# Kernel tuning notes

Measured on AMD Instinct MI355X. Metric: run time of the kernel, lower is better.

The kernel has to match this reference:

```python
import jax, jax.numpy as jnp
import numpy as np

B, P, D, H, U, C = 32, 196, 512, 8, 4, 500

def setup_inputs() -> dict:
    key = jax.random.key(0)
    ks = jax.random.split(key, 12)
    s = 0.02
    return {
        "patch_embeddings": jax.random.normal(ks[0], (B, P, D), jnp.float32),
        "global_features": jax.random.normal(ks[1], (B, D), jnp.float32),
        "query_vectors": jax.random.normal(ks[2], (H, D), jnp.float32) * s,
        "dom_W": jax.random.normal(ks[3], (D, D), jnp.float32) / np.sqrt(D),
        "dom_b": jnp.zeros((D,), jnp.float32),
        "sem_W": jax.random.normal(ks[4], (H, D, D), jnp.float32) / np.sqrt(D),
        "sem_b": jnp.zeros((H, D), jnp.float32),
        "unknown_semantic_tokens": jax.random.normal(ks[5], (U, D), jnp.float32) * s,
        "known_prefix": jax.random.normal(ks[6], (C, 1, D), jnp.float32) * s,   # SOS embedding per class
        "known_suffix": jax.random.normal(ks[7], (C, 1, D), jnp.float32) * s,   # last-token embedding per class
        "unk_prefix": jax.random.normal(ks[8], (1, D), jnp.float32) * s,
        "unk_suffix": jax.random.normal(ks[9], (1, D), jnp.float32) * s,
    }


def reference(patch_embeddings, global_features, query_vectors, dom_W, dom_b,
              sem_W, sem_b, unknown_semantic_tokens, known_prefix, known_suffix,
              unk_prefix, unk_suffix):
    b, p, d = patch_embeddings.shape
    h = query_vectors.shape[0]
    c = known_prefix.shape[0]
    u = unknown_semantic_tokens.shape[0]

    # SemanticTokenExtractor: per-head attention over patches (vectorized over heads)
    scores = jnp.einsum('bpd,hd->bph', patch_embeddings, query_vectors)      # [B,P,H]
    weights = jax.nn.softmax(scores, axis=1)                                  # softmax over patches
    semantic_tokens = jnp.einsum('bph,bpd->bhd', weights, patch_embeddings)   # [B,H,D]

    # DomainTokenGenerator (2D input -> identity) + domain projection (torch Linear: x @ W.T + b)
    projected_domain = global_features @ dom_W.T + dom_b                      # [B,D]

    # Per-head semantic projections: head k uses its own Linear
    projected_sem = jnp.einsum('bhd,hed->bhe', semantic_tokens, sem_W) + sem_b  # [B,H,D]

    # Known prompts: for each (b, c): [prefix_c(1), domain_b(1), semantics_b(H), suffix_c(1)]
    pre = jnp.broadcast_to(known_prefix[None], (b, c, 1, d))
    dom = jnp.broadcast_to(projected_domain[:, None, None, :], (b, c, 1, d))
    sem = jnp.broadcast_to(projected_sem[:, None], (b, c, h, d))
    suf = jnp.broadcast_to(known_suffix[None], (b, c, 1, d))
    known_prompts = jnp.concatenate([pre, dom, sem, suf], axis=2).reshape(b * c, h + 3, d)

    # Unknown prompts: [unk_prefix(1), domain_b(1), unknown_semantic_tokens(U), unk_suffix(1)]
    upre = jnp.broadcast_to(unk_prefix[None], (b, 1, d))
    udom = projected_domain[:, None, :]
    usem = jnp.broadcast_to(unknown_semantic_tokens[None], (b, u, d))
    usuf = jnp.broadcast_to(unk_suffix[None], (b, 1, d))
    unknown_prompts = jnp.concatenate([upre, udom, usem, usuf], axis=1)       # [B, U+3, D]

    return known_prompts, unknown_prompts, semantic_tokens
```

## Files before the change

kernel.cpp:

```cpp
#include <hip/hip_runtime.h>

typedef unsigned int uint32;
typedef uint32 v4u __attribute__((ext_vector_type(4)));

#define Bb 32
#define Pp 196
#define Dd 512
#define Hh 8
#define Uu 4
#define Cc 500

#define OUT1_ELEM_OFF 90112000
#define OUT2_ELEM_OFF 90226688

#define NPC 16

#define WS_SC   0
#define WS_PART 51200
#define WS_DOM  2148352
#define WS_SEM  2164736

__device__ __forceinline__ float dot4(float4 a, float4 b, float acc) {
    acc = fmaf(a.x, b.x, acc);
    acc = fmaf(a.y, b.y, acc);
    acc = fmaf(a.z, b.z, acc);
    acc = fmaf(a.w, b.w, acc);
    return acc;
}

__global__ __launch_bounds__(256)
void k_scores(const float* __restrict__ patch, const float* __restrict__ query,
              float* __restrict__ sc) {
    __shared__ float s_q[Hh * Dd];
    const int b = blockIdx.x / 49;
    const int p0 = (blockIdx.x % 49) * 4;
    const int tid = threadIdx.x;
    for (int j = tid; j < Hh * Dd / 4; j += 256)
        ((float4*)s_q)[j] = ((const float4*)query)[j];
    __syncthreads();

    const int wave = tid >> 6, lane = tid & 63;
    const int p = p0 + wave;
    const float* pr = patch + ((size_t)b * Pp + p) * Dd + lane * 8;
    const float4 v0 = *(const float4*)pr;
    const float4 v1 = *(const float4*)(pr + 4);

    float out = 0.f;
#pragma unroll
    for (int h = 0; h < 8; ++h) {
        const float4 q0 = *(const float4*)&s_q[h * Dd + lane * 8];
        const float4 q1 = *(const float4*)&s_q[h * Dd + lane * 8 + 4];
        float a = dot4(v0, q0, 0.f);
        a = dot4(v1, q1, a);
#pragma unroll
        for (int m = 32; m >= 1; m >>= 1) a += __shfl_xor(a, m, 64);
        if (lane == h) out = a;
    }
    if (lane < 8) sc[((size_t)b * Hh + lane) * Pp + p] = out;
}

__global__ __launch_bounds__(256)
void k_pool_part(const float* __restrict__ patch, const float* __restrict__ sc,
                 float* __restrict__ part) {
    __shared__ float s_w[Hh * Pp];
    const int b = blockIdx.x >> 4;
    const int pc = blockIdx.x & 15;
    const int tid = threadIdx.x;

    for (int j = tid; j < Hh * Pp; j += 256) s_w[j] = sc[(size_t)b * Hh * Pp + j];
    __syncthreads();

    {
        const int h = tid >> 5, gl = tid & 31;
        float m = -1e30f;
        for (int p = gl; p < Pp; p += 32) m = fmaxf(m, s_w[h * Pp + p]);
#pragma unroll
        for (int mm = 16; mm >= 1; mm >>= 1) m = fmaxf(m, __shfl_xor(m, mm, 64));
        float s = 0.f;
        for (int p = gl; p < Pp; p += 32) s += __expf(s_w[h * Pp + p] - m);
#pragma unroll
        for (int mm = 16; mm >= 1; mm >>= 1) s += __shfl_xor(s, mm, 64);
        const float inv = 1.f / s;
        for (int p = gl; p < Pp; p += 32)
            s_w[h * Pp + p] = __expf(s_w[h * Pp + p] - m) * inv;
    }
    __syncthreads();

    const int f = tid & 127;
    const int hq = tid >> 7;
    const int pstart = pc * 13;
    const int pend = (pstart + 13 < Pp) ? pstart + 13 : Pp;
    float4 a0 = {0, 0, 0, 0}, a1 = a0, a2 = a0, a3 = a0;
    const float4* pb4 = (const float4*)(patch + (size_t)b * Pp * Dd);
    for (int p = pstart; p < pend; ++p) {
        const float4 pv = pb4[p * 128 + f];
        const float w0 = s_w[(hq * 4 + 0) * Pp + p];
        const float w1 = s_w[(hq * 4 + 1) * Pp + p];
        const float w2 = s_w[(hq * 4 + 2) * Pp + p];
        const float w3 = s_w[(hq * 4 + 3) * Pp + p];
        a0.x = fmaf(w0, pv.x, a0.x); a0.y = fmaf(w0, pv.y, a0.y);
        a0.z = fmaf(w0, pv.z, a0.z); a0.w = fmaf(w0, pv.w, a0.w);
        a1.x = fmaf(w1, pv.x, a1.x); a1.y = fmaf(w1, pv.y, a1.y);
        a1.z = fmaf(w1, pv.z, a1.z); a1.w = fmaf(w1, pv.w, a1.w);
        a2.x = fmaf(w2, pv.x, a2.x); a2.y = fmaf(w2, pv.y, a2.y);
        a2.z = fmaf(w2, pv.z, a2.z); a2.w = fmaf(w2, pv.w, a2.w);
        a3.x = fmaf(w3, pv.x, a3.x); a3.y = fmaf(w3, pv.y, a3.y);
        a3.z = fmaf(w3, pv.z, a3.z); a3.w = fmaf(w3, pv.w, a3.w);
    }
    float4* po = (float4*)part + ((size_t)b * NPC + pc) * 1024;
    po[(hq * 4 + 0) * 128 + f] = a0;
    po[(hq * 4 + 1) * 128 + f] = a1;
    po[(hq * 4 + 2) * 128 + f] = a2;
    po[(hq * 4 + 3) * 128 + f] = a3;
}

__global__ __launch_bounds__(256)
void k_combine(const float* __restrict__ part, float* __restrict__ st) {
    const int idx = blockIdx.x * 256 + threadIdx.x;
    const int b = idx >> 10;
    const int r = idx & 1023;
    const float4* p4 = (const float4*)part;
    float4 a = {0, 0, 0, 0};
#pragma unroll
    for (int pc = 0; pc < NPC; ++pc) {
        const float4 v = p4[((size_t)b * NPC + pc) * 1024 + r];
        a.x += v.x; a.y += v.y; a.z += v.z; a.w += v.w;
    }
    ((float4*)st)[idx] = a;
}

#define PJS 513
__global__ __launch_bounds__(256)
void k_proj(const float* __restrict__ gf, const float* __restrict__ domW,
            const float* __restrict__ domb, const float* __restrict__ semW,
            const float* __restrict__ semb, const float* __restrict__ st,
            float* __restrict__ dom_ws, float* __restrict__ sem_ws) {
    __shared__ float s_w[32 * PJS];
    __shared__ float s_st[32 * PJS];
    const int blk = blockIdx.x;
    const int tid = threadIdx.x;
    if (blk < 128) {
        const int h = blk >> 4;
        const int e0 = (blk & 15) * 32;
        for (int g = tid; g < 32 * 128; g += 256) {
            const int r = g >> 7, c4 = g & 127;
            const float4 w = ((const float4*)semW)[((size_t)(h * Dd + e0 + r)) * 128 + c4];
            float* dw = &s_w[r * PJS + c4 * 4];
            dw[0] = w.x; dw[1] = w.y; dw[2] = w.z; dw[3] = w.w;
            const float4 s = ((const float4*)st)[((size_t)(r * Hh + h)) * 128 + c4];
            float* ds = &s_st[r * PJS + c4 * 4];
            ds[0] = s.x; ds[1] = s.y; ds[2] = s.z; ds[3] = s.w;
        }
        __syncthreads();
        const int pe = tid & 15;
        const int pb = tid >> 4;
        const float* w0r = &s_w[(2 * pe) * PJS];
        const float* w1r = &s_w[(2 * pe + 1) * PJS];
        const float* s0r = &s_st[(2 * pb) * PJS];
        const float* s1r = &s_st[(2 * pb + 1) * PJS];
        float a00 = 0.f, a01 = 0.f, a10 = 0.f, a11 = 0.f;
#pragma unroll 8
        for (int d = 0; d < Dd; ++d) {
            const float w0 = w0r[d], w1 = w1r[d];
            const float s0 = s0r[d], s1 = s1r[d];
            a00 = fmaf(s0, w0, a00);
            a01 = fmaf(s0, w1, a01);
            a10 = fmaf(s1, w0, a10);
            a11 = fmaf(s1, w1, a11);
        }
        const int e_ = e0 + 2 * pe;
        const float b0 = semb[h * Dd + e_], b1 = semb[h * Dd + e_ + 1];
        float* o0 = &sem_ws[((2 * pb) * Hh + h) * Dd + e_];
        float* o1 = &sem_ws[((2 * pb + 1) * Hh + h) * Dd + e_];
        o0[0] = a00 + b0; o0[1] = a01 + b1;
        o1[0] = a10 + b0; o1[1] = a11 + b1;
    } else {
        const int tg = (blk - 128) * 256 + tid;
        const int b = tg >> 9;
        const int e = tg & 511;
        const float4* wr = (const float4*)(domW + (size_t)e * Dd);
        const float4* gr = (const float4*)(gf + (size_t)b * Dd);
        float acc = domb[e];
#pragma unroll 8
        for (int j = 0; j < Dd / 4; ++j) acc = dot4(gr[j], wr[j], acc);
        dom_ws[b * Dd + e] = acc;
    }
}

__global__ __launch_bounds__(256)
void k_assemble(const v4u* __restrict__ pre, const v4u* __restrict__ suf,
                const v4u* __restrict__ dom, const v4u* __restrict__ sem,
                const v4u* __restrict__ upre, const v4u* __restrict__ usuf,
                const v4u* __restrict__ ust,
                v4u* __restrict__ out0, v4u* __restrict__ out1) {
    const int blk = blockIdx.x;
    const int tid = threadIdx.x;
    if (blk < 16000) {
        const int b = blk / 500;
        const int c = blk % 500;
        v4u* row = out0 + (size_t)blk * 1408;
#pragma unroll
        for (int k = 0; k < 6; ++k) {
            const int i = tid + k * 256;
            if (k < 5 || i < 1408) {
                const int t = i >> 7;
                const int off = i & 127;
                v4u v;
                if (t == 0) v = pre[c * 128 + off];
                else if (t == 10) v = suf[c * 128 + off];
                else if (t == 1) v = dom[b * 128 + off];
                else v = sem[b * 1024 + (t - 2) * 128 + off];
                row[i] = v;
            }
        }
    } else {
        const int b = blk - 16000;
#pragma unroll
        for (int k = 0; k < 4; ++k) {
            const int i = tid + k * 256;
            if (k < 3 || i < 896) {
                const int t = i >> 7;
                const int off = i & 127;
                v4u v;
                if (t == 0) v = upre[off];
                else if (t == 6) v = usuf[off];
                else if (t == 1) v = dom[b * 128 + off];
                else v = ust[(t - 2) * 128 + off];
                out1[b * 896 + i] = v;
            }
        }
    }
}

extern "C" void kernel_launch(void* const* d_in, const int* in_sizes, int n_in,
                              void* d_out, int out_size, void* d_ws, size_t ws_size,
                              hipStream_t stream) {
    const float* patch = (const float*)d_in[0];
    const float* gf    = (const float*)d_in[1];
    const float* query = (const float*)d_in[2];
    const float* domW  = (const float*)d_in[3];
    const float* domb  = (const float*)d_in[4];
    const float* semW  = (const float*)d_in[5];
    const float* semb  = (const float*)d_in[6];
    const float* ust   = (const float*)d_in[7];
    const float* pre   = (const float*)d_in[8];
    const float* suf   = (const float*)d_in[9];
    const float* upre  = (const float*)d_in[10];
    const float* usuf  = (const float*)d_in[11];

    float* out = (float*)d_out;
    float* st_out = out + OUT2_ELEM_OFF;

    float* ws   = (float*)d_ws;
    float* sc_w = ws + WS_SC;
    float* part = ws + WS_PART;
    float* domp = ws + WS_DOM;
    float* semp = ws + WS_SEM;

    hipLaunchKernelGGL(k_scores, dim3(Bb * 49), dim3(256), 0, stream, patch, query, sc_w);
    hipLaunchKernelGGL(k_pool_part, dim3(Bb * NPC), dim3(256), 0, stream, patch, sc_w, part);
    hipLaunchKernelGGL(k_combine, dim3(128), dim3(256), 0, stream, part, st_out);
    hipLaunchKernelGGL(k_proj, dim3(192), dim3(256), 0, stream,
                       gf, domW, domb, semW, semb, st_out, domp, semp);
    hipLaunchKernelGGL(k_assemble, dim3(16032), dim3(256), 0, stream,
                       (const v4u*)pre, (const v4u*)suf,
                       (const v4u*)domp, (const v4u*)semp,
                       (const v4u*)upre, (const v4u*)usuf, (const v4u*)ust,
                       (v4u*)out, (v4u*)(out + OUT1_ELEM_OFF));
}
```

Baseline: 435.3 us.

## Batch classes per assemble block with shared token cache and nontemporal stores

Each k_assemble block now writes ten class rows for one batch element, staging the shared domain and semantic tokens in LDS once instead of re-reading them from global memory for every row. All output writes use nontemporal stores so the very large prompt output does not pollute the cache. k_proj separately switches to float4 LDS stores and reads with padded row stride 516 and a strided output mapping, vectorizing its inner dot products. The assemble grid drops from 16032 to 1632 blocks, which reduces parallelism per block but amortizes index math and token loads.

```diff
diff --git a/kernel.cpp b/kernel.cpp
--- a/kernel.cpp
+++ b/kernel.cpp
@@ -129,7 +129,7 @@
     ((float4*)st)[idx] = a;
 }
 
-#define PJS 513
+#define PJS 516
 __global__ __launch_bounds__(256)
 void k_proj(const float* __restrict__ gf, const float* __restrict__ domW,
             const float* __restrict__ domb, const float* __restrict__ semW,
@@ -145,35 +145,35 @@
         for (int g = tid; g < 32 * 128; g += 256) {
             const int r = g >> 7, c4 = g & 127;
             const float4 w = ((const float4*)semW)[((size_t)(h * Dd + e0 + r)) * 128 + c4];
-            float* dw = &s_w[r * PJS + c4 * 4];
-            dw[0] = w.x; dw[1] = w.y; dw[2] = w.z; dw[3] = w.w;
+            *(float4*)&s_w[r * PJS + c4 * 4] = w;
             const float4 s = ((const float4*)st)[((size_t)(r * Hh + h)) * 128 + c4];
-            float* ds = &s_st[r * PJS + c4 * 4];
-            ds[0] = s.x; ds[1] = s.y; ds[2] = s.z; ds[3] = s.w;
+            *(float4*)&s_st[r * PJS + c4 * 4] = s;
         }
         __syncthreads();
         const int pe = tid & 15;
         const int pb = tid >> 4;
-        const float* w0r = &s_w[(2 * pe) * PJS];
-        const float* w1r = &s_w[(2 * pe + 1) * PJS];
-        const float* s0r = &s_st[(2 * pb) * PJS];
-        const float* s1r = &s_st[(2 * pb + 1) * PJS];
+        const float* w0r = &s_w[pe * PJS];
+        const float* w1r = &s_w[(pe + 16) * PJS];
+        const float* s0r = &s_st[pb * PJS];
+        const float* s1r = &s_st[(pb + 16) * PJS];
         float a00 = 0.f, a01 = 0.f, a10 = 0.f, a11 = 0.f;
-#pragma unroll 8
-        for (int d = 0; d < Dd; ++d) {
-            const float w0 = w0r[d], w1 = w1r[d];
-            const float s0 = s0r[d], s1 = s1r[d];
-            a00 = fmaf(s0, w0, a00);
-            a01 = fmaf(s0, w1, a01);
-            a10 = fmaf(s1, w0, a10);
-            a11 = fmaf(s1, w1, a11);
-        }
-        const int e_ = e0 + 2 * pe;
-        const float b0 = semb[h * Dd + e_], b1 = semb[h * Dd + e_ + 1];
-        float* o0 = &sem_ws[((2 * pb) * Hh + h) * Dd + e_];
-        float* o1 = &sem_ws[((2 * pb + 1) * Hh + h) * Dd + e_];
-        o0[0] = a00 + b0; o0[1] = a01 + b1;
-        o1[0] = a10 + b0; o1[1] = a11 + b1;
+#pragma unroll 4
+        for (int d = 0; d < Dd; d += 4) {
+            const float4 w0 = *(const float4*)&w0r[d];
+            const float4 w1 = *(const float4*)&w1r[d];
+            const float4 s0 = *(const float4*)&s0r[d];
+            const float4 s1 = *(const float4*)&s1r[d];
+            a00 = dot4(s0, w0, a00);
+            a01 = dot4(s0, w1, a01);
+            a10 = dot4(s1, w0, a10);
+            a11 = dot4(s1, w1, a11);
+        }
+        const int e_ = e0 + pe;
+        const float b0 = semb[h * Dd + e_], b1 = semb[h * Dd + e_ + 16];
+        sem_ws[((size_t)pb * Hh + h) * Dd + e_]             = a00 + b0;
+        sem_ws[((size_t)pb * Hh + h) * Dd + e_ + 16]        = a01 + b1;
+        sem_ws[((size_t)(pb + 16) * Hh + h) * Dd + e_]      = a10 + b0;
+        sem_ws[((size_t)(pb + 16) * Hh + h) * Dd + e_ + 16] = a11 + b1;
     } else {
         const int tg = (blk - 128) * 256 + tid;
         const int b = tg >> 9;
@@ -187,34 +187,42 @@
     }
 }
 
+#define KN_CB 10
 __global__ __launch_bounds__(256)
 void k_assemble(const v4u* __restrict__ pre, const v4u* __restrict__ suf,
                 const v4u* __restrict__ dom, const v4u* __restrict__ sem,
                 const v4u* __restrict__ upre, const v4u* __restrict__ usuf,
                 const v4u* __restrict__ ust,
                 v4u* __restrict__ out0, v4u* __restrict__ out1) {
+    __shared__ v4u s_tok[1152];
     const int blk = blockIdx.x;
     const int tid = threadIdx.x;
-    if (blk < 16000) {
-        const int b = blk / 500;
-        const int c = blk % 500;
-        v4u* row = out0 + (size_t)blk * 1408;
-#pragma unroll
-        for (int k = 0; k < 6; ++k) {
-            const int i = tid + k * 256;
-            if (k < 5 || i < 1408) {
-                const int t = i >> 7;
-                const int off = i & 127;
-                v4u v;
-                if (t == 0) v = pre[c * 128 + off];
-                else if (t == 10) v = suf[c * 128 + off];
-                else if (t == 1) v = dom[b * 128 + off];
-                else v = sem[b * 1024 + (t - 2) * 128 + off];
-                row[i] = v;
+    if (blk < Bb * (Cc / KN_CB)) {
+        const int b = blk / (Cc / KN_CB);
+        const int c0 = (blk % (Cc / KN_CB)) * KN_CB;
+        for (int j = tid; j < 1152; j += 256)
+            s_tok[j] = (j < 128) ? dom[b * 128 + j] : sem[b * 1024 + (j - 128)];
+        __syncthreads();
+#pragma unroll
+        for (int cj = 0; cj < KN_CB; ++cj) {
+            const int c = c0 + cj;
+            v4u* row = out0 + (size_t)(b * Cc + c) * 1408;
+#pragma unroll
+            for (int k = 0; k < 6; ++k) {
+                const int i = tid + k * 256;
+                if (k < 5 || i < 1408) {
+                    const int t = i >> 7;
+                    const int off = i & 127;
+                    v4u v;
+                    if (t == 0) v = pre[c * 128 + off];
+                    else if (t == 10) v = suf[c * 128 + off];
+                    else v = s_tok[(t - 1) * 128 + off];
+                    __builtin_nontemporal_store(v, &row[i]);
+                }
             }
         }
     } else {
-        const int b = blk - 16000;
+        const int b = blk - Bb * (Cc / KN_CB);
 #pragma unroll
         for (int k = 0; k < 4; ++k) {
             const int i = tid + k * 256;
@@ -226,7 +234,7 @@
                 else if (t == 6) v = usuf[off];
                 else if (t == 1) v = dom[b * 128 + off];
                 else v = ust[(t - 2) * 128 + off];
-                out1[b * 896 + i] = v;
+                __builtin_nontemporal_store(v, &out1[b * 896 + i]);
             }
         }
     }
@@ -262,7 +270,7 @@
     hipLaunchKernelGGL(k_combine, dim3(128), dim3(256), 0, stream, part, st_out);
     hipLaunchKernelGGL(k_proj, dim3(192), dim3(256), 0, stream,
                        gf, domW, domb, semW, semb, st_out, domp, semp);
-    hipLaunchKernelGGL(k_assemble, dim3(16032), dim3(256), 0, stream,
+    hipLaunchKernelGGL(k_assemble, dim3(Bb * (Cc / KN_CB) + Bb), dim3(256), 0, stream,
                        (const v4u*)pre, (const v4u*)suf,
                        (const v4u*)domp, (const v4u*)semp,
                        (const v4u*)upre, (const v4u*)usuf, (const v4u*)ust,
```

Result: no change. 438.2 us (+0.7%).
